# Kernel tuning notes

Measured on AMD Instinct MI355X. Metric: run time of the kernel, lower is better.

Reference implementation:

```python
import jax, jax.numpy as jnp
import numpy as np

D = 768  # hidden dim hard-coded in the module


def setup_inputs() -> dict:
    key = jax.random.key(0)
    k1, k2, k3, k4, k5 = jax.random.split(key, 5)
    N, M = 512, 512
    return {
        "text_output": jax.random.normal(k1, (N, D), dtype=jnp.float32),
        "visual_output": jax.random.normal(k2, (M, D), dtype=jnp.float32),
        "W1": jax.random.normal(k3, (D, D), dtype=jnp.float32),
        "W2": jax.random.normal(k4, (D, D), dtype=jnp.float32),
        "W3": jax.random.normal(k5, (D, D), dtype=jnp.float32),
    }


def reference(text_output, visual_output, W1, W2, W3):
    # C[n,m] = tanh( (text @ W1) . visual[m] )
    C = jnp.tanh((text_output @ W1) @ visual_output.T)            # (N, M)
    W2_text = text_output @ W2                                    # (N, D)
    W3_visual = visual_output @ W3.T                              # (M, D)
    # M[n,m,:] = tanh(W2_text[n] + W3_visual[m] * C[n,m])
    Mt = jnp.tanh(W2_text[:, None, :] + W3_visual[None, :, :] * C[..., None])  # (N, M, D)
    # score[n,m] = text[n] . M[n,m]  (replaces the per-row Python loop)
    score = jnp.einsum("nd,nmd->nm", text_output, Mt)             # (N, M)
    return score
```

## Files before the change

### kernel.cpp

```cpp
#include <hip/hip_runtime.h>

#define DD   768
#define NN   512
#define MM   512

#define PRE_K 2.88539008177792681472f

typedef _Float16 h8 __attribute__((ext_vector_type(8)));
typedef __attribute__((ext_vector_type(4))) float f32x4;

__device__ __forceinline__ float fexp(float x) { return __builtin_amdgcn_exp2f(x); }
__device__ __forceinline__ float frcp(float x) { return __builtin_amdgcn_rcpf(x); }
__device__ __forceinline__ float fast_tanh(float x) {
  return 1.0f - 2.0f * frcp(fexp(PRE_K * x) + 1.0f);
}

__device__ __forceinline__ void splitf(float x, ushort& h, ushort& l) {
  const _Float16 hh = (_Float16)x;
  const _Float16 ll = (_Float16)(x - (float)hh);
  h = __builtin_bit_cast(unsigned short, hh);
  l = __builtin_bit_cast(unsigned short, ll);
}

__global__ __launch_bounds__(256) void prep_kernel(
    const float* __restrict__ text, const float* __restrict__ visual,
    const float* __restrict__ W1, const float* __restrict__ W2,
    const float* __restrict__ W3,
    ushort* __restrict__ th, ushort* __restrict__ tl,
    ushort* __restrict__ vh, ushort* __restrict__ vl,
    ushort* __restrict__ w3h, ushort* __restrict__ w3l,
    ushort* __restrict__ w1th, ushort* __restrict__ w1tl,
    ushort* __restrict__ w2th, ushort* __restrict__ w2tl,
    float* __restrict__ out)
{
  __shared__ float Lt[32][33];
  const int b = blockIdx.x;
  const int t = threadIdx.x;

  if (b < 1344) {
    const float* src; ushort *dh, *dl; size_t off;
    if (b < 384)      { src = text;   dh = th;  dl = tl;  off = (size_t)b * 1024; }
    else if (b < 768) { src = visual; dh = vh;  dl = vl;  off = (size_t)(b - 384) * 1024; }
    else              { src = W3;     dh = w3h; dl = w3l; off = (size_t)(b - 768) * 1024; }
    const size_t i = off + (size_t)t * 4;
    const float4 v = *(const float4*)&src[i];
    ushort4 h, l;
    splitf(v.x, h.x, l.x); splitf(v.y, h.y, l.y);
    splitf(v.z, h.z, l.z); splitf(v.w, h.w, l.w);
    *(ushort4*)&dh[i] = h;
    *(ushort4*)&dl[i] = l;
  } else if (b < 2496) {
    const int tt = b - 1344;
    const bool second = tt >= 576;
    const int tile = second ? tt - 576 : tt;
    const float* W = second ? W2 : W1;
    ushort* oh = second ? w2th : w1th;
    ushort* ol = second ? w2tl : w1tl;
    const int k0 = (tile / 24) * 32, j0 = (tile % 24) * 32;
    {
      const int k = t >> 3, j4 = (t & 7) * 4;
      const float4 v = *(const float4*)&W[(size_t)(k0 + k) * DD + j0 + j4];
      Lt[j4 + 0][k] = v.x; Lt[j4 + 1][k] = v.y;
      Lt[j4 + 2][k] = v.z; Lt[j4 + 3][k] = v.w;
    }
    __syncthreads();
    {
      const int j = t >> 3, k4 = (t & 7) * 4;
      ushort4 h, l;
      splitf(Lt[j][k4 + 0], h.x, l.x); splitf(Lt[j][k4 + 1], h.y, l.y);
      splitf(Lt[j][k4 + 2], h.z, l.z); splitf(Lt[j][k4 + 3], h.w, l.w);
      *(ushort4*)&oh[(size_t)(j0 + j) * DD + k0 + k4] = h;
      *(ushort4*)&ol[(size_t)(j0 + j) * DD + k0 + k4] = l;
    }
  } else {
    float* red = (float*)Lt;
    const int u = b - 2496;
    const int n0 = u * 2;
    const int half = t >> 7;
    const int lt = t & 127;

    const float* tr = text + (size_t)(n0 + half) * DD;
    float s = 0.f;
    #pragma unroll
    for (int i = 0; i < DD / 128; ++i) s += tr[lt + i * 128];
    red[t] = s;
    __syncthreads();
    #pragma unroll
    for (int st = 64; st > 0; st >>= 1) {
      if (lt < st) red[t] += red[t + st];
      __syncthreads();
    }
    const float Tn = red[half << 7];
    float4 o; o.x = Tn; o.y = Tn; o.z = Tn; o.w = Tn;
    *(float4*)&out[(size_t)(n0 + half) * MM + lt * 4] = o;
  }
}

#define BK2   64
#define LROW2 72
#define APL2  (32 * LROW2)
#define BPL2  (64 * LROW2)

template <bool ALO>
__device__ __forceinline__ void gemm_core64(
    ushort* __restrict__ As, ushort* __restrict__ Bs,
    const ushort* __restrict__ Ahg, const ushort* __restrict__ Alg,
    const ushort* __restrict__ Bhg, const ushort* __restrict__ Blg,
    int i0, int j0, int k0, int nsteps, f32x4* acc)
{
  const int tid  = threadIdx.x;
  const int arow = tid >> 3;
  const int ks8  = (tid & 7) * 8;
  const size_t ga  = (size_t)(i0 + arow) * DD + k0 + ks8;
  const size_t gb0 = (size_t)(j0 + arow) * DD + k0 + ks8;
  const size_t gb1 = (size_t)(j0 + arow + 32) * DD + k0 + ks8;
  const int lwa  = arow * LROW2 + ks8;
  const int lwb0 = arow * LROW2 + ks8;
  const int lwb1 = (arow + 32) * LROW2 + ks8;

  const int lane = tid & 63, wave = tid >> 6;
  const int r15 = lane & 15, quad = lane >> 4;
  const int wr = wave >> 1, wc = wave & 1;
  const int fa = (wr * 16 + r15) * LROW2 + quad * 8;
  const int fb = (wc * 32 + r15) * LROW2 + quad * 8;

  h8 pah = *(const h8*)(Ahg + ga);
  h8 pal; if (ALO) pal = *(const h8*)(Alg + ga);
  h8 pbh0 = *(const h8*)(Bhg + gb0);
  h8 pbh1 = *(const h8*)(Bhg + gb1);
  h8 pbl0 = *(const h8*)(Blg + gb0);
  h8 pbl1 = *(const h8*)(Blg + gb1);

  int p = 0;
  *(h8*)&As[lwa] = pah;
  if (ALO) *(h8*)&As[APL2 + lwa] = pal;
  *(h8*)&Bs[lwb0] = pbh0; *(h8*)&Bs[lwb1] = pbh1;
  *(h8*)&Bs[BPL2 + lwb0] = pbl0; *(h8*)&Bs[BPL2 + lwb1] = pbl1;
  __syncthreads();

  for (int s = 0; s < nsteps; ++s) {
    const bool more = (s + 1 < nsteps);
    if (more) {
      pah = *(const h8*)(Ahg + ga + (s + 1) * BK2);
      if (ALO) pal = *(const h8*)(Alg + ga + (s + 1) * BK2);
      pbh0 = *(const h8*)(Bhg + gb0 + (s + 1) * BK2);
      pbh1 = *(const h8*)(Bhg + gb1 + (s + 1) * BK2);
      pbl0 = *(const h8*)(Blg + gb0 + (s + 1) * BK2);
      pbl1 = *(const h8*)(Blg + gb1 + (s + 1) * BK2);
    }
    ushort* Ac = As + p * 2 * APL2;
    ushort* Bc = Bs + p * 2 * BPL2;
    #pragma unroll
    for (int kk = 0; kk < 2; ++kk) {
      const int fo = kk * 32;
      const h8 a_h = *(const h8*)&Ac[fa + fo];
      h8 a_l; if (ALO) a_l = *(const h8*)&Ac[APL2 + fa + fo];
      h8 b_h[2], b_l[2];
      #pragma unroll
      for (int c = 0; c < 2; ++c) {
        b_h[c] = *(const h8*)&Bc[fb + c * 16 * LROW2 + fo];
        b_l[c] = *(const h8*)&Bc[BPL2 + fb + c * 16 * LROW2 + fo];
      }
      #pragma unroll
      for (int c = 0; c < 2; ++c)
        acc[c] = __builtin_amdgcn_mfma_f32_16x16x32_f16(a_h, b_h[c], acc[c], 0, 0, 0);
      #pragma unroll
      for (int c = 0; c < 2; ++c)
        acc[c] = __builtin_amdgcn_mfma_f32_16x16x32_f16(a_h, b_l[c], acc[c], 0, 0, 0);
      if (ALO) {
        #pragma unroll
        for (int c = 0; c < 2; ++c)
          acc[c] = __builtin_amdgcn_mfma_f32_16x16x32_f16(a_l, b_h[c], acc[c], 0, 0, 0);
      }
    }
    if (more) {
      const int q = p ^ 1;
      ushort* An = As + q * 2 * APL2;
      ushort* Bn = Bs + q * 2 * BPL2;
      *(h8*)&An[lwa] = pah;
      if (ALO) *(h8*)&An[APL2 + lwa] = pal;
      *(h8*)&Bn[lwb0] = pbh0; *(h8*)&Bn[lwb1] = pbh1;
      *(h8*)&Bn[BPL2 + lwb0] = pbl0; *(h8*)&Bn[BPL2 + lwb1] = pbl1;
    }
    __syncthreads();
    p ^= 1;
  }
}

__global__ __launch_bounds__(256) void mfma1_kernel(
    const ushort* __restrict__ th, const ushort* __restrict__ tl,
    const ushort* __restrict__ vh, const ushort* __restrict__ vl,
    const ushort* __restrict__ w1th, const ushort* __restrict__ w1tl,
    const ushort* __restrict__ w2th, const ushort* __restrict__ w2tl,
    const ushort* __restrict__ w3h, const ushort* __restrict__ w3l,
    ushort* __restrict__ Ah, ushort* __restrict__ Al,
    float* __restrict__ kw2t, float* __restrict__ kw3v)
{
  __shared__ ushort As[2 * 2 * APL2];
  __shared__ ushort Bs[2 * 2 * BPL2];

  const int z  = blockIdx.z;
  const int j0 = blockIdx.x * 64;
  const int i0 = blockIdx.y * 32;

  f32x4 acc[2];
  acc[0] = (f32x4){0.f, 0.f, 0.f, 0.f};
  acc[1] = (f32x4){0.f, 0.f, 0.f, 0.f};

  if (z == 0)
    gemm_core64<true >(As, Bs, th, tl, w1th, w1tl, i0, j0, 0, DD / BK2, acc);
  else if (z == 1)
    gemm_core64<false>(As, Bs, th, tl, w2th, w2tl, i0, j0, 0, DD / BK2, acc);
  else
    gemm_core64<false>(As, Bs, vh, vl, w3h,  w3l,  i0, j0, 0, DD / BK2, acc);

  const int lane = threadIdx.x & 63, wave = threadIdx.x >> 6;
  const int r15 = lane & 15, quad = lane >> 4;
  const int wr = wave >> 1, wc = wave & 1;
  if (z == 0) {
    #pragma unroll
    for (int c = 0; c < 2; ++c)
      #pragma unroll
      for (int r = 0; r < 4; ++r) {
        const size_t o = (size_t)(i0 + wr * 16 + quad * 4 + r) * DD
                       + j0 + wc * 32 + c * 16 + r15;
        splitf(acc[c][r], Ah[o], Al[o]);
      }
  } else {
    float* Out = (z == 1) ? kw2t : kw3v;
    #pragma unroll
    for (int c = 0; c < 2; ++c)
      #pragma unroll
      for (int r = 0; r < 4; ++r)
        Out[(size_t)(i0 + wr * 16 + quad * 4 + r) * DD + j0 + wc * 32 + c * 16 + r15] =
            acc[c][r] * PRE_K;
  }
}

__global__ __launch_bounds__(256) void mfma2_kernel(
    const ushort* __restrict__ Ah, const ushort* __restrict__ Al,
    const ushort* __restrict__ vh, const ushort* __restrict__ vl,
    float* __restrict__ Q)
{
  __shared__ ushort As[2 * 2 * APL2];
  __shared__ ushort Bs[2 * 2 * BPL2];

  const int z  = blockIdx.z;
  const int j0 = blockIdx.x * 64;
  const int i0 = blockIdx.y * 32;

  f32x4 acc[2];
  acc[0] = (f32x4){0.f, 0.f, 0.f, 0.f};
  acc[1] = (f32x4){0.f, 0.f, 0.f, 0.f};
  gemm_core64<true>(As, Bs, Ah, Al, vh, vl, i0, j0, z * (DD / 4), (DD / 4) / BK2, acc);

  const int lane = threadIdx.x & 63, wave = threadIdx.x >> 6;
  const int r15 = lane & 15, quad = lane >> 4;
  const int wr = wave >> 1, wc = wave & 1;
  float* Qp = Q + (size_t)z * NN * MM;
  #pragma unroll
  for (int c = 0; c < 2; ++c)
    #pragma unroll
    for (int r = 0; r < 4; ++r)
      Qp[(size_t)(i0 + wr * 16 + quad * 4 + r) * MM + j0 + wc * 32 + c * 16 + r15] =
          acc[c][r];
}

#define DCH    32
#define DRANGE 192
#define MLDW   36

__global__ __launch_bounds__(256, 4) void main_kernel(
    const float* __restrict__ text, const float* __restrict__ kw2t,
    const float* __restrict__ kw3v, const float* __restrict__ Q,
    float* __restrict__ out)
{
  __shared__ float sbuf[2][64 * MLDW];

  const int tid = threadIdx.x;
  const int nl = tid >> 4;
  const int ml = tid & 15;
  const int n0 = blockIdx.y * 16;
  const int m0 = blockIdx.x * 32;
  const int z  = blockIdx.z;
  const int n  = n0 + nl;
  const int mA = m0 + ml, mB = mA + 16;
  const int dbase = z * DRANGE;

  float cA = 0.f, cB = 0.f;
  #pragma unroll
  for (int zz = 0; zz < 4; ++zz) {
    const float* q = Q + (size_t)zz * NN * MM + (size_t)n * MM;
    cA += q[mA]; cB += q[mB];
  }
  cA = fast_tanh(cA); cB = fast_tanh(cB);

  float4 aA = {0.f, 0.f, 0.f, 0.f};
  float4 aB = {0.f, 0.f, 0.f, 0.f};

  const int srow = tid >> 3;
  const int sc   = (tid & 7) << 2;
  const float* g1 = (srow < 16)
      ? &text[(size_t)(n0 + srow) * DD + dbase + sc]
      : &kw2t[(size_t)(n0 + srow - 16) * DD + dbase + sc];
  const float* g3 = &kw3v[(size_t)(m0 + srow) * DD + dbase + sc];
  const int w1 = srow * MLDW + sc;
  const int w3 = (32 + srow) * MLDW + sc;

  float4 r1 = *(const float4*)g1;
  float4 r3 = *(const float4*)g3;
  int p = 0;
  *(float4*)&sbuf[0][w1] = r1;
  *(float4*)&sbuf[0][w3] = r3;
  __syncthreads();

  #pragma unroll
  for (int c = 0; c < DRANGE / DCH; ++c) {
    const bool more = (c + 1 < DRANGE / DCH);
    if (more) {
      r1 = *(const float4*)(g1 + (c + 1) * DCH);
      r3 = *(const float4*)(g3 + (c + 1) * DCH);
    }
    const float* bp = sbuf[p];
    #pragma unroll 4
    for (int j = 0; j < DCH; j += 4) {
      const float4 tv  = *(const float4*)&bp[nl * MLDW + j];
      const float4 w2v = *(const float4*)&bp[(16 + nl) * MLDW + j];
      const float4 w3A = *(const float4*)&bp[(32 + ml) * MLDW + j];
      const float4 w3B = *(const float4*)&bp[(48 + ml) * MLDW + j];
      aA.x = fmaf(tv.x, frcp(fexp(fmaf(w3A.x, cA, w2v.x)) + 1.0f), aA.x);
      aA.y = fmaf(tv.y, frcp(fexp(fmaf(w3A.y, cA, w2v.y)) + 1.0f), aA.y);
      aA.z = fmaf(tv.z, frcp(fexp(fmaf(w3A.z, cA, w2v.z)) + 1.0f), aA.z);
      aA.w = fmaf(tv.w, frcp(fexp(fmaf(w3A.w, cA, w2v.w)) + 1.0f), aA.w);
      aB.x = fmaf(tv.x, frcp(fexp(fmaf(w3B.x, cB, w2v.x)) + 1.0f), aB.x);
      aB.y = fmaf(tv.y, frcp(fexp(fmaf(w3B.y, cB, w2v.y)) + 1.0f), aB.y);
      aB.z = fmaf(tv.z, frcp(fexp(fmaf(w3B.z, cB, w2v.z)) + 1.0f), aB.z);
      aB.w = fmaf(tv.w, frcp(fexp(fmaf(w3B.w, cB, w2v.w)) + 1.0f), aB.w);
    }
    if (more) {
      const int q = p ^ 1;
      *(float4*)&sbuf[q][w1] = r1;
      *(float4*)&sbuf[q][w3] = r3;
    }
    __syncthreads();
    p ^= 1;
  }

  float* op = out + (size_t)n * MM;
  unsafeAtomicAdd(&op[mA], -2.0f * ((aA.x + aA.y) + (aA.z + aA.w)));
  unsafeAtomicAdd(&op[mB], -2.0f * ((aB.x + aB.y) + (aB.z + aB.w)));
}

extern "C" void kernel_launch(void* const* d_in, const int* in_sizes, int n_in,
                              void* d_out, int out_size, void* d_ws, size_t ws_size,
                              hipStream_t stream) {
  const float* text   = (const float*)d_in[0];
  const float* visual = (const float*)d_in[1];
  const float* W1     = (const float*)d_in[2];
  const float* W2     = (const float*)d_in[3];
  const float* W3     = (const float*)d_in[4];
  float* out = (float*)d_out;

  char* base = (char*)d_ws;
  ushort* th   = (ushort*)(base);
  ushort* tl   = (ushort*)(base + 786432);
  ushort* vh   = (ushort*)(base + 1572864);
  ushort* vl   = (ushort*)(base + 2359296);
  ushort* w1th = (ushort*)(base + 3145728);
  ushort* w1tl = (ushort*)(base + 4325376);
  ushort* w2th = (ushort*)(base + 5505024);
  ushort* w2tl = (ushort*)(base + 6684672);
  ushort* w3h  = (ushort*)(base + 7864320);
  ushort* w3l  = (ushort*)(base + 9043968);
  ushort* Ah   = (ushort*)(base + 10223616);
  ushort* Al   = (ushort*)(base + 11010048);
  float*  kw2t = (float*) (base + 11796480);
  float*  kw3v = (float*) (base + 13369344);
  float*  Q    = (float*) (base + 3145728);

  hipLaunchKernelGGL(prep_kernel, dim3(2752), dim3(256), 0, stream,
                     text, visual, W1, W2, W3,
                     th, tl, vh, vl, w3h, w3l, w1th, w1tl, w2th, w2tl, out);
  hipLaunchKernelGGL(mfma1_kernel, dim3(DD / 64, NN / 32, 3), dim3(256), 0, stream,
                     th, tl, vh, vl, w1th, w1tl, w2th, w2tl, w3h, w3l,
                     Ah, Al, kw2t, kw3v);
  hipLaunchKernelGGL(mfma2_kernel, dim3(MM / 64, NN / 32, 4), dim3(256), 0, stream,
                     Ah, Al, vh, vl, Q);
  hipLaunchKernelGGL(main_kernel, dim3(MM / 32, NN / 16, 4), dim3(256), 0, stream,
                     text, kw2t, kw3v, Q, out);
}
```

Before: 133.0 us.

## Fuse fp16 hi/lo split and transpose into GEMM loaders, drop prep kernel

Removes the separate prep kernel that split fp32 inputs into fp16 hi/lo pairs and transposed W1/W2 into workspace. The GEMM cores now load fp32 directly, split in registers, and for W1/W2 transpose through an extra shared-memory tile, which adds a barrier per k-step. The row-sum initialisation of the output moves into extra blocks of mfma2. This saves one launch and the workspace round trip, but adds split work and a synchronisation inside every GEMM block.

Result: slower. 136.5 us (+2.7%).

```diff
diff --git a/kernel.cpp b/kernel.cpp
--- a/kernel.cpp
+++ b/kernel.cpp
@@ -22,132 +22,138 @@
   l = __builtin_bit_cast(unsigned short, ll);
 }
 
-__global__ __launch_bounds__(256) void prep_kernel(
-    const float* __restrict__ text, const float* __restrict__ visual,
-    const float* __restrict__ W1, const float* __restrict__ W2,
-    const float* __restrict__ W3,
-    ushort* __restrict__ th, ushort* __restrict__ tl,
-    ushort* __restrict__ vh, ushort* __restrict__ vl,
-    ushort* __restrict__ w3h, ushort* __restrict__ w3l,
-    ushort* __restrict__ w1th, ushort* __restrict__ w1tl,
-    ushort* __restrict__ w2th, ushort* __restrict__ w2tl,
-    float* __restrict__ out)
-{
-  __shared__ float Lt[32][33];
-  const int b = blockIdx.x;
-  const int t = threadIdx.x;
-
-  if (b < 1344) {
-    const float* src; ushort *dh, *dl; size_t off;
-    if (b < 384)      { src = text;   dh = th;  dl = tl;  off = (size_t)b * 1024; }
-    else if (b < 768) { src = visual; dh = vh;  dl = vl;  off = (size_t)(b - 384) * 1024; }
-    else              { src = W3;     dh = w3h; dl = w3l; off = (size_t)(b - 768) * 1024; }
-    const size_t i = off + (size_t)t * 4;
-    const float4 v = *(const float4*)&src[i];
-    ushort4 h, l;
-    splitf(v.x, h.x, l.x); splitf(v.y, h.y, l.y);
-    splitf(v.z, h.z, l.z); splitf(v.w, h.w, l.w);
-    *(ushort4*)&dh[i] = h;
-    *(ushort4*)&dl[i] = l;
-  } else if (b < 2496) {
-    const int tt = b - 1344;
-    const bool second = tt >= 576;
-    const int tile = second ? tt - 576 : tt;
-    const float* W = second ? W2 : W1;
-    ushort* oh = second ? w2th : w1th;
-    ushort* ol = second ? w2tl : w1tl;
-    const int k0 = (tile / 24) * 32, j0 = (tile % 24) * 32;
-    {
-      const int k = t >> 3, j4 = (t & 7) * 4;
-      const float4 v = *(const float4*)&W[(size_t)(k0 + k) * DD + j0 + j4];
-      Lt[j4 + 0][k] = v.x; Lt[j4 + 1][k] = v.y;
-      Lt[j4 + 2][k] = v.z; Lt[j4 + 3][k] = v.w;
-    }
-    __syncthreads();
-    {
-      const int j = t >> 3, k4 = (t & 7) * 4;
-      ushort4 h, l;
-      splitf(Lt[j][k4 + 0], h.x, l.x); splitf(Lt[j][k4 + 1], h.y, l.y);
-      splitf(Lt[j][k4 + 2], h.z, l.z); splitf(Lt[j][k4 + 3], h.w, l.w);
-      *(ushort4*)&oh[(size_t)(j0 + j) * DD + k0 + k4] = h;
-      *(ushort4*)&ol[(size_t)(j0 + j) * DD + k0 + k4] = l;
-    }
-  } else {
-    float* red = (float*)Lt;
-    const int u = b - 2496;
-    const int n0 = u * 2;
-    const int half = t >> 7;
-    const int lt = t & 127;
-
-    const float* tr = text + (size_t)(n0 + half) * DD;
-    float s = 0.f;
-    #pragma unroll
-    for (int i = 0; i < DD / 128; ++i) s += tr[lt + i * 128];
-    red[t] = s;
-    __syncthreads();
-    #pragma unroll
-    for (int st = 64; st > 0; st >>= 1) {
-      if (lt < st) red[t] += red[t + st];
-      __syncthreads();
-    }
-    const float Tn = red[half << 7];
-    float4 o; o.x = Tn; o.y = Tn; o.z = Tn; o.w = Tn;
-    *(float4*)&out[(size_t)(n0 + half) * MM + lt * 4] = o;
-  }
+__device__ __forceinline__ void split4(const float4 v, ushort4& h, ushort4& l) {
+  splitf(v.x, h.x, l.x); splitf(v.y, h.y, l.y);
+  splitf(v.z, h.z, l.z); splitf(v.w, h.w, l.w);
 }
 
 #define BK2   64
 #define LROW2 72
 #define APL2  (32 * LROW2)
 #define BPL2  (64 * LROW2)
-
-template <bool ALO>
-__device__ __forceinline__ void gemm_core64(
-    ushort* __restrict__ As, ushort* __restrict__ Bs,
+#define TPAD  68
+
+template <bool ALO, bool AF32, int BKIND>
+__device__ __forceinline__ void gemm_core64u(
+    ushort* __restrict__ As, ushort* __restrict__ Bs, float* __restrict__ Ts,
+    const float* __restrict__ Af,
     const ushort* __restrict__ Ahg, const ushort* __restrict__ Alg,
-    const ushort* __restrict__ Bhg, const ushort* __restrict__ Blg,
+    const float* __restrict__ Bf,
     int i0, int j0, int k0, int nsteps, f32x4* acc)
 {
-  const int tid  = threadIdx.x;
-  const int arow = tid >> 3;
-  const int ks8  = (tid & 7) * 8;
-  const size_t ga  = (size_t)(i0 + arow) * DD + k0 + ks8;
-  const size_t gb0 = (size_t)(j0 + arow) * DD + k0 + ks8;
-  const size_t gb1 = (size_t)(j0 + arow + 32) * DD + k0 + ks8;
-  const int lwa  = arow * LROW2 + ks8;
-  const int lwb0 = arow * LROW2 + ks8;
-  const int lwb1 = (arow + 32) * LROW2 + ks8;
-
+  const int tid = threadIdx.x;
   const int lane = tid & 63, wave = tid >> 6;
   const int r15 = lane & 15, quad = lane >> 4;
   const int wr = wave >> 1, wc = wave & 1;
   const int fa = (wr * 16 + r15) * LROW2 + quad * 8;
   const int fb = (wc * 32 + r15) * LROW2 + quad * 8;
 
-  h8 pah = *(const h8*)(Ahg + ga);
-  h8 pal; if (ALO) pal = *(const h8*)(Alg + ga);
-  h8 pbh0 = *(const h8*)(Bhg + gb0);
-  h8 pbh1 = *(const h8*)(Bhg + gb1);
-  h8 pbl0 = *(const h8*)(Blg + gb0);
-  h8 pbl1 = *(const h8*)(Blg + gb1);
+  const int arow = tid >> 3;
+  const int ks8  = (tid & 7) * 8;
+  const int lwa  = arow * LROW2 + ks8;
+  const size_t ga  = (size_t)(i0 + arow) * DD + k0 + ks8;
+  const size_t gb0 = (size_t)(j0 + arow) * DD + k0 + ks8;
+  const size_t gb1 = (size_t)(j0 + arow + 32) * DD + k0 + ks8;
+  const int lwb0 = arow * LROW2 + ks8;
+  const int lwb1 = (arow + 32) * LROW2 + ks8;
+  const int kt  = tid >> 4;
+  const int j4  = (tid & 15) * 4;
+  const int tj  = tid >> 2;
+  const int tkc = (tid & 3) * 16;
+
+  float4 a0, a1; h8 pah, pal;
+  float4 b0a, b0b, b1a, b1b;
+  float4 w0, w1, w2, w3;
+
+  auto loadS = [&](int s) {
+    if constexpr (AF32) {
+      a0 = *(const float4*)&Af[ga + (size_t)s * BK2];
+      a1 = *(const float4*)&Af[ga + (size_t)s * BK2 + 4];
+    } else {
+      pah = *(const h8*)(Ahg + ga + (size_t)s * BK2);
+      if (ALO) pal = *(const h8*)(Alg + ga + (size_t)s * BK2);
+    }
+    if constexpr (BKIND == 1) {
+      b0a = *(const float4*)&Bf[gb0 + (size_t)s * BK2];
+      b0b = *(const float4*)&Bf[gb0 + (size_t)s * BK2 + 4];
+      b1a = *(const float4*)&Bf[gb1 + (size_t)s * BK2];
+      b1b = *(const float4*)&Bf[gb1 + (size_t)s * BK2 + 4];
+    } else {
+      const size_t kb = (size_t)(k0 + s * BK2);
+      w0 = *(const float4*)&Bf[(kb + kt)      * DD + j0 + j4];
+      w1 = *(const float4*)&Bf[(kb + kt + 16) * DD + j0 + j4];
+      w2 = *(const float4*)&Bf[(kb + kt + 32) * DD + j0 + j4];
+      w3 = *(const float4*)&Bf[(kb + kt + 48) * DD + j0 + j4];
+    }
+  };
+
+  auto stageA = [&](ushort* dst) {
+    if constexpr (AF32) {
+      ushort4 h0, l0, h1, l1;
+      split4(a0, h0, l0); split4(a1, h1, l1);
+      *(ushort4*)&dst[lwa]     = h0;
+      *(ushort4*)&dst[lwa + 4] = h1;
+      if (ALO) {
+        *(ushort4*)&dst[APL2 + lwa]     = l0;
+        *(ushort4*)&dst[APL2 + lwa + 4] = l1;
+      }
+    } else {
+      *(h8*)&dst[lwa] = pah;
+      if (ALO) *(h8*)&dst[APL2 + lwa] = pal;
+    }
+  };
+
+  auto stageB1 = [&](ushort* dst) {
+    ushort4 h0, l0, h1, l1;
+    split4(b0a, h0, l0); split4(b0b, h1, l1);
+    *(ushort4*)&dst[lwb0]            = h0;
+    *(ushort4*)&dst[lwb0 + 4]        = h1;
+    *(ushort4*)&dst[BPL2 + lwb0]     = l0;
+    *(ushort4*)&dst[BPL2 + lwb0 + 4] = l1;
+    split4(b1a, h0, l0); split4(b1b, h1, l1);
+    *(ushort4*)&dst[lwb1]            = h0;
+    *(ushort4*)&dst[lwb1 + 4]        = h1;
+    *(ushort4*)&dst[BPL2 + lwb1]     = l0;
+    *(ushort4*)&dst[BPL2 + lwb1 + 4] = l1;
+  };
+
+  auto stageTs = [&]() {
+    *(float4*)&Ts[(kt)      * TPAD + j4] = w0;
+    *(float4*)&Ts[(kt + 16) * TPAD + j4] = w1;
+    *(float4*)&Ts[(kt + 32) * TPAD + j4] = w2;
+    *(float4*)&Ts[(kt + 48) * TPAD + j4] = w3;
+  };
+
+  auto phase2 = [&](ushort* dst) {
+    ushort* db = &dst[tj * LROW2 + tkc];
+    ushort* dl = db + BPL2;
+    #pragma unroll
+    for (int c4 = 0; c4 < 4; ++c4) {
+      const int kb = tkc + c4 * 4;
+      ushort4 h, l;
+      splitf(Ts[(kb + 0) * TPAD + tj], h.x, l.x);
+      splitf(Ts[(kb + 1) * TPAD + tj], h.y, l.y);
+      splitf(Ts[(kb + 2) * TPAD + tj], h.z, l.z);
+      splitf(Ts[(kb + 3) * TPAD + tj], h.w, l.w);
+      *(ushort4*)&db[c4 * 4] = h;
+      *(ushort4*)&dl[c4 * 4] = l;
+    }
+  };
+
+  loadS(0);
+  stageA(As);
+  if constexpr (BKIND == 1) stageB1(Bs);
+  else {
+    stageTs();
+    __syncthreads();
+    phase2(Bs);
+  }
+  __syncthreads();
 
   int p = 0;
-  *(h8*)&As[lwa] = pah;
-  if (ALO) *(h8*)&As[APL2 + lwa] = pal;
-  *(h8*)&Bs[lwb0] = pbh0; *(h8*)&Bs[lwb1] = pbh1;
-  *(h8*)&Bs[BPL2 + lwb0] = pbl0; *(h8*)&Bs[BPL2 + lwb1] = pbl1;
-  __syncthreads();
-
   for (int s = 0; s < nsteps; ++s) {
     const bool more = (s + 1 < nsteps);
-    if (more) {
-      pah = *(const h8*)(Ahg + ga + (s + 1) * BK2);
-      if (ALO) pal = *(const h8*)(Alg + ga + (s + 1) * BK2);
-      pbh0 = *(const h8*)(Bhg + gb0 + (s + 1) * BK2);
-      pbh1 = *(const h8*)(Bhg + gb1 + (s + 1) * BK2);
-      pbl0 = *(const h8*)(Blg + gb0 + (s + 1) * BK2);
-      pbl1 = *(const h8*)(Blg + gb1 + (s + 1) * BK2);
-    }
+    if (more) loadS(s + 1);
     ushort* Ac = As + p * 2 * APL2;
     ushort* Bc = Bs + p * 2 * BPL2;
     #pragma unroll
@@ -173,14 +179,16 @@
           acc[c] = __builtin_amdgcn_mfma_f32_16x16x32_f16(a_l, b_h[c], acc[c], 0, 0, 0);
       }
     }
+    ushort* An = As + (p ^ 1) * 2 * APL2;
+    ushort* Bn = Bs + (p ^ 1) * 2 * BPL2;
     if (more) {
-      const int q = p ^ 1;
-      ushort* An = As + q * 2 * APL2;
-      ushort* Bn = Bs + q * 2 * BPL2;
-      *(h8*)&An[lwa] = pah;
-      if (ALO) *(h8*)&An[APL2 + lwa] = pal;
-      *(h8*)&Bn[lwb0] = pbh0; *(h8*)&Bn[lwb1] = pbh1;
-      *(h8*)&Bn[BPL2 + lwb0] = pbl0; *(h8*)&Bn[BPL2 + lwb1] = pbl1;
+      stageA(An);
+      if constexpr (BKIND == 1) stageB1(Bn);
+      else stageTs();
+    }
+    if constexpr (BKIND == 2) {
+      __syncthreads();
+      if (more) phase2(Bn);
     }
     __syncthreads();
     p ^= 1;
@@ -188,16 +196,15 @@
 }
 
 __global__ __launch_bounds__(256) void mfma1_kernel(
-    const ushort* __restrict__ th, const ushort* __restrict__ tl,
-    const ushort* __restrict__ vh, const ushort* __restrict__ vl,
-    const ushort* __restrict__ w1th, const ushort* __restrict__ w1tl,
-    const ushort* __restrict__ w2th, const ushort* __restrict__ w2tl,
-    const ushort* __restrict__ w3h, const ushort* __restrict__ w3l,
+    const float* __restrict__ text, const float* __restrict__ visual,
+    const float* __restrict__ W1, const float* __restrict__ W2,
+    const float* __restrict__ W3,
     ushort* __restrict__ Ah, ushort* __restrict__ Al,
     float* __restrict__ kw2t, float* __restrict__ kw3v)
 {
   __shared__ ushort As[2 * 2 * APL2];
   __shared__ ushort Bs[2 * 2 * BPL2];
+  __shared__ float  Ts[64 * TPAD];
 
   const int z  = blockIdx.z;
   const int j0 = blockIdx.x * 64;
@@ -208,11 +215,14 @@
   acc[1] = (f32x4){0.f, 0.f, 0.f, 0.f};
 
   if (z == 0)
-    gemm_core64<true >(As, Bs, th, tl, w1th, w1tl, i0, j0, 0, DD / BK2, acc);
+    gemm_core64u<true,  true, 2>(As, Bs, Ts, text,   nullptr, nullptr, W1,
+                                 i0, j0, 0, DD / BK2, acc);
   else if (z == 1)
-    gemm_core64<false>(As, Bs, th, tl, w2th, w2tl, i0, j0, 0, DD / BK2, acc);
+    gemm_core64u<false, true, 2>(As, Bs, Ts, text,   nullptr, nullptr, W2,
+                                 i0, j0, 0, DD / BK2, acc);
   else
-    gemm_core64<false>(As, Bs, vh, vl, w3h,  w3l,  i0, j0, 0, DD / BK2, acc);
+    gemm_core64u<false, true, 1>(As, Bs, Ts, visual, nullptr, nullptr, W3,
+                                 i0, j0, 0, DD / BK2, acc);
 
   const int lane = threadIdx.x & 63, wave = threadIdx.x >> 6;
   const int r15 = lane & 15, quad = lane >> 4;
@@ -239,12 +249,40 @@
 
 __global__ __launch_bounds__(256) void mfma2_kernel(
     const ushort* __restrict__ Ah, const ushort* __restrict__ Al,
-    const ushort* __restrict__ vh, const ushort* __restrict__ vl,
-    float* __restrict__ Q)
+    const float* __restrict__ visual, const float* __restrict__ text,
+    float* __restrict__ Q, float* __restrict__ out)
 {
   __shared__ ushort As[2 * 2 * APL2];
   __shared__ ushort Bs[2 * 2 * BPL2];
 
+  const int t = threadIdx.x;
+  if (blockIdx.z == 4) {
+    float* red = (float*)As;
+    const int bid  = blockIdx.y * 8 + blockIdx.x;
+    const int half = t >> 7;
+    const int lt   = t & 127;
+    #pragma unroll
+    for (int u2 = 0; u2 < 2; ++u2) {
+      const int n0 = (bid + 128 * u2) * 2;
+      const float* tr = text + (size_t)(n0 + half) * DD;
+      float s = 0.f;
+      #pragma unroll
+      for (int i = 0; i < DD / 128; ++i) s += tr[lt + i * 128];
+      red[t] = s;
+      __syncthreads();
+      #pragma unroll
+      for (int st = 64; st > 0; st >>= 1) {
+        if (lt < st) red[t] += red[t + st];
+        __syncthreads();
+      }
+      const float Tn = red[half << 7];
+      float4 o; o.x = Tn; o.y = Tn; o.z = Tn; o.w = Tn;
+      *(float4*)&out[(size_t)(n0 + half) * MM + lt * 4] = o;
+      __syncthreads();
+    }
+    return;
+  }
+
   const int z  = blockIdx.z;
   const int j0 = blockIdx.x * 64;
   const int i0 = blockIdx.y * 32;
@@ -252,9 +290,10 @@
   f32x4 acc[2];
   acc[0] = (f32x4){0.f, 0.f, 0.f, 0.f};
   acc[1] = (f32x4){0.f, 0.f, 0.f, 0.f};
-  gemm_core64<true>(As, Bs, Ah, Al, vh, vl, i0, j0, z * (DD / 4), (DD / 4) / BK2, acc);
-
-  const int lane = threadIdx.x & 63, wave = threadIdx.x >> 6;
+  gemm_core64u<true, false, 1>(As, Bs, nullptr, nullptr, Ah, Al, visual,
+                               i0, j0, z * (DD / 4), (DD / 4) / BK2, acc);
+
+  const int lane = t & 63, wave = t >> 6;
   const int r15 = lane & 15, quad = lane >> 4;
   const int wr = wave >> 1, wc = wave & 1;
   float* Qp = Q + (size_t)z * NN * MM;
@@ -362,30 +401,16 @@
   float* out = (float*)d_out;
 
   char* base = (char*)d_ws;
-  ushort* th   = (ushort*)(base);
-  ushort* tl   = (ushort*)(base + 786432);
-  ushort* vh   = (ushort*)(base + 1572864);
-  ushort* vl   = (ushort*)(base + 2359296);
-  ushort* w1th = (ushort*)(base + 3145728);
-  ushort* w1tl = (ushort*)(base + 4325376);
-  ushort* w2th = (ushort*)(base + 5505024);
-  ushort* w2tl = (ushort*)(base + 6684672);
-  ushort* w3h  = (ushort*)(base + 7864320);
-  ushort* w3l  = (ushort*)(base + 9043968);
-  ushort* Ah   = (ushort*)(base + 10223616);
-  ushort* Al   = (ushort*)(base + 11010048);
-  float*  kw2t = (float*) (base + 11796480);
-  float*  kw3v = (float*) (base + 13369344);
-  float*  Q    = (float*) (base + 3145728);
-
-  hipLaunchKernelGGL(prep_kernel, dim3(2752), dim3(256), 0, stream,
-                     text, visual, W1, W2, W3,
-                     th, tl, vh, vl, w3h, w3l, w1th, w1tl, w2th, w2tl, out);
+  ushort* Ah   = (ushort*)(base);
+  ushort* Al   = (ushort*)(base + 786432);
+  float*  kw2t = (float*) (base + 1572864);
+  float*  kw3v = (float*) (base + 3145728);
+  float*  Q    = (float*) (base + 4718592);
+
   hipLaunchKernelGGL(mfma1_kernel, dim3(DD / 64, NN / 32, 3), dim3(256), 0, stream,
-                     th, tl, vh, vl, w1th, w1tl, w2th, w2tl, w3h, w3l,
-                     Ah, Al, kw2t, kw3v);
-  hipLaunchKernelGGL(mfma2_kernel, dim3(MM / 64, NN / 32, 4), dim3(256), 0, stream,
-                     Ah, Al, vh, vl, Q);
+                     text, visual, W1, W2, W3, Ah, Al, kw2t, kw3v);
+  hipLaunchKernelGGL(mfma2_kernel, dim3(MM / 64, NN / 32, 5), dim3(256), 0, stream,
+                     Ah, Al, visual, text, Q, out);
   hipLaunchKernelGGL(main_kernel, dim3(MM / 32, NN / 16, 4), dim3(256), 0, stream,
                      text, kw2t, kw3v, Q, out);
 }
```
